# Kernel tuning notes

Measured on AMD Instinct MI355X. Metric: run time of the kernel, lower is better.

## Reference

```python
import jax, jax.numpy as jnp
import numpy as np

N_NODES = 100000


def gcn_layer(x, ei, W, b):
    # PyG GCNConv with add_self_loops=True, edge_weight=None (all ones)
    N = x.shape[0]
    loops = jnp.arange(N, dtype=ei.dtype)
    src = jnp.concatenate([ei[0], loops])
    dst = jnp.concatenate([ei[1], loops])
    h = x @ W  # [N, out_dim]
    ones = jnp.ones(src.shape[0], dtype=x.dtype)
    deg = jax.ops.segment_sum(ones, dst, num_segments=N)
    dinv = jnp.where(deg > 0, jax.lax.rsqrt(deg), 0.0)
    norm = dinv[src] * dinv[dst]  # [E+N]
    msgs = norm[:, None] * h[src]
    out = jax.ops.segment_sum(msgs, dst, num_segments=N)
    return out + b


def forward_once(x, ei, W1, b1, W2, b2):
    h = jax.nn.relu(gcn_layer(x, ei, W1, b1))
    # Dropout(0.25) is identity in eval mode
    z = gcn_layer(h, ei, W2, b2)
    return z  # [N, embed_dim]


def setup_inputs() -> dict:
    key = jax.random.key(0)
    k = jax.random.split(key, 6)
    feat_dim, hidden_dim, embed_dim = 128, 32, 16
    R, E = 4, 1600000
    x = jax.random.normal(k[0], (N_NODES, feat_dim), dtype=jnp.float32)
    eis = jax.random.randint(k[1], (R, 2, E), 0, N_NODES, dtype=jnp.int32)
    s1 = 1.0 / np.sqrt(feat_dim)
    s2 = 1.0 / np.sqrt(hidden_dim)
    W1 = jax.random.uniform(k[2], (feat_dim, hidden_dim), jnp.float32, -s1, s1)
    b1 = jax.random.uniform(k[3], (hidden_dim,), jnp.float32, -s1, s1)
    W2 = jax.random.uniform(k[4], (hidden_dim, embed_dim), jnp.float32, -s2, s2)
    b2 = jax.random.uniform(k[5], (embed_dim,), jnp.float32, -s2, s2)
    return {"x": x, "eis": eis, "W1": W1, "b1": b1, "W2": W2, "b2": b2}


def reference(x, eis, W1, b1, W2, b2):
    # vectorize the per-relation loop over the leading R axis of eis
    embeds = jax.vmap(lambda ei: forward_once(x, ei, W1, b1, W2, b2))(eis)
    # default reduce: embeds.sum(dim=2) on [R, N, embed_dim] -> [R, N]
    return embeds.sum(axis=2)
```

## Files before the change

### kernel.cpp

```cpp
#include <hip/hip_runtime.h>


constexpr int N    = 100000;
constexpr int E    = 1600000;
constexpr int R    = 4;
constexpr int FEAT = 128;
constexpr int HID  = 32;
constexpr int EMB  = 16;
constexpr int M    = R * N;
constexpr int BS   = 256;
constexpr int SH    = 9;
constexpr int BSPAN = 1 << SH;
constexpr int NBUCK = (N + BSPAN - 1) / BSPAN;
constexpr int CH    = 4096;
constexpr int EPT   = CH / BS;
constexpr int NBKr  = (E + CH - 1) / CH;
constexpr int RB    = R * NBUCK;
constexpr int CAP   = 8960;
constexpr int SPT   = (CAP + BSPAN - 1) / BSPAN;
constexpr int FIX   = 16;
constexpr int GNB   = 64;
constexpr int XPITCH = 132;

typedef _Float16 half8 __attribute__((ext_vector_type(8)));
typedef _Float16 half2v __attribute__((ext_vector_type(2)));

__global__ __launch_bounds__(BS)
void k_gemm_h0(const float* __restrict__ x, const float* __restrict__ W1,
               _Float16* __restrict__ H0h) {
    __shared__ float xs[GNB * XPITCH];
    int base = blockIdx.x * GNB;
    int tid  = threadIdx.x;
#pragma unroll
    for (int u = 0; u < 8; ++u) {
        int f = tid + u * BS;
        int n = f >> 5;
        int c = f & 31;
        if (base + n < N) {
            float4 v = ((const float4*)(x + (size_t)(base + n) * FEAT))[c];
            int p = c ^ ((n & 7) << 2);
            *(float4*)&xs[n * XPITCH + p * 4] = v;
        }
    }
    __syncthreads();
    int oct = __builtin_amdgcn_readfirstlane(tid >> 6);
    int l   = tid & 63;
    int i   = base + l;
    const float* wp = W1 + oct * 8;
    float acc[8];
#pragma unroll
    for (int kk = 0; kk < 8; ++kk) acc[kk] = 0.f;
#pragma unroll 4
    for (int c = 0; c < 32; ++c) {
        int p = c ^ ((l & 7) << 2);
        float4 xv = *(const float4*)&xs[l * XPITCH + p * 4];
        float xk[4] = {xv.x, xv.y, xv.z, xv.w};
#pragma unroll
        for (int dk = 0; dk < 4; ++dk) {
            const float* wr = wp + (c * 4 + dk) * HID;
#pragma unroll
            for (int j = 0; j < 8; ++j)
                acc[j] = fmaf(xk[dk], wr[j], acc[j]);
        }
    }
    half8 hv;
#pragma unroll
    for (int kk = 0; kk < 8; ++kk) hv[kk] = (_Float16)acc[kk];
    if (i < N) ((half8*)H0h)[i * 4 + oct] = hv;
}

__global__ void k_wrow(const float* __restrict__ W2, const float* __restrict__ b2,
                       float* __restrict__ wrowbuf, _Float16* __restrict__ Hsc) {
    int j = threadIdx.x;
    if (j < HID) {
        float s = 0.f;
#pragma unroll
        for (int k = 0; k < EMB; ++k) s += W2[j * EMB + k];
        wrowbuf[j] = s;
    } else if (j == HID) {
        float s = 0.f;
#pragma unroll
        for (int k = 0; k < EMB; ++k) s += b2[k];
        wrowbuf[HID] = s;
    } else if (j >= 34 && j < 50) {
        ((unsigned*)(Hsc + (size_t)M * HID))[j - 34] = 0u;
    }
}

__global__ void k_scat2(const int* __restrict__ eis, int* __restrict__ gcur,
                        int* __restrict__ binned) {
    __shared__ int hist[NBUCK], lstart[NBUCK], cursor[NBUCK], gbase[NBUCK];
    __shared__ int wpart[BS / 64];
    __shared__ int shuf[CH];
    __shared__ unsigned char bkt[CH];
    int r = blockIdx.x / NBKr, k = blockIdx.x - r * NBKr;
    const int* srcp = eis + (size_t)r * 2 * E;
    const int* dstp = srcp + E;
    int e0 = k * CH, n = min(CH, E - e0);
    int tid = threadIdx.x;

    int dreg[EPT], sreg[EPT];
    if (n == CH) {
#pragma unroll
        for (int u = 0; u < EPT; ++u) {
            dreg[u] = dstp[e0 + tid + u * BS];
            sreg[u] = srcp[e0 + tid + u * BS];
        }
    } else {
#pragma unroll
        for (int u = 0; u < EPT; ++u) {
            int i = tid + u * BS;
            dreg[u] = (i < n) ? dstp[e0 + i] : -1;
            sreg[u] = (i < n) ? srcp[e0 + i] : 0;
        }
    }
    for (int b = tid; b < NBUCK; b += BS) hist[b] = 0;
    __syncthreads();
#pragma unroll
    for (int u = 0; u < EPT; ++u)
        if (dreg[u] >= 0) atomicAdd(&hist[dreg[u] >> SH], 1);
    __syncthreads();
    int v = (tid < NBUCK) ? hist[tid] : 0;
    int lanei = tid & 63;
    int s = v;
#pragma unroll
    for (int d = 1; d < 64; d <<= 1) {
        int xup = __shfl_up(s, d, 64);
        s += (lanei >= d) ? xup : 0;
    }
    if (lanei == 63) wpart[tid >> 6] = s;
    __syncthreads();
    int offw = 0;
#pragma unroll
    for (int ww = 0; ww < BS / 64; ++ww)
        offw += (ww < (tid >> 6)) ? wpart[ww] : 0;
    int ex = offw + s - v;
    if (tid < NBUCK) {
        lstart[tid] = ex;
        cursor[tid] = ex;
        gbase[tid] = atomicAdd(&gcur[r * NBUCK + tid], v);
    }
    __syncthreads();
#pragma unroll
    for (int u = 0; u < EPT; ++u) {
        int d = dreg[u];
        if (d >= 0) {
            int b = d >> SH;
            int pos = atomicAdd(&cursor[b], 1);
            shuf[pos] = ((d & (BSPAN - 1)) << 17) | sreg[u];
            bkt[pos]  = (unsigned char)b;
        }
    }
    __syncthreads();
    for (int i = tid; i < n; i += BS) {
        int b = bkt[i];
        int pos = gbase[b] + (i - lstart[b]);
        if (pos < CAP)
            binned[(size_t)(r * NBUCK + b) * CAP + pos] = shuf[i];
    }
}

__global__ __launch_bounds__(BSPAN)
void k_sort3(const int* __restrict__ gcur, int* __restrict__ binned,
             int* __restrict__ off, int* __restrict__ cnt,
             float* __restrict__ dinv, const half8* __restrict__ H0h,
             half8* __restrict__ Hsc, int* __restrict__ fixedsrc) {
    __shared__ int fix_lds[FIX * BSPAN];
    __shared__ int hist[BSPAN], cur[BSPAN], exs[BSPAN];
    __shared__ int wpart[BSPAN / 64];
    int gb = blockIdx.x;
    int r = gb / NBUCK, b = gb - r * NBUCK;
    int n = min(gcur[gb], CAP);
    int base = gb * CAP;
    int tid = threadIdx.x;
    int rg[SPT];
#pragma unroll
    for (int u = 0; u < SPT; ++u) {
        int i = tid + u * BSPAN;
        rg[u] = (i < n) ? binned[base + i] : -1;
    }
    hist[tid] = 0;
    __syncthreads();
#pragma unroll
    for (int u = 0; u < SPT; ++u)
        if (rg[u] >= 0) atomicAdd(&hist[((unsigned)rg[u]) >> 17], 1);
    __syncthreads();
    int v = hist[tid];
    int lanei = tid & 63;
    int s = v;
#pragma unroll
    for (int d = 1; d < 64; d <<= 1) {
        int xup = __shfl_up(s, d, 64);
        s += (lanei >= d) ? xup : 0;
    }
    if (lanei == 63) wpart[tid >> 6] = s;
    __syncthreads();
    int offw = 0;
#pragma unroll
    for (int ww = 0; ww < BSPAN / 64; ++ww)
        offw += (ww < (tid >> 6)) ? wpart[ww] : 0;
    int ex = offw + s - v;
    cur[tid] = ex;
    exs[tid] = ex;
    int node = (b << SH) + tid;
    int ri = r * N + node;
    if (node < N) {
        off[ri] = base + ex;
        cnt[ri] = v;
        dinv[ri] = rsqrtf((float)v + 1.0f);
    }
    __syncthreads();
#pragma unroll
    for (int u = 0; u < SPT; ++u) {
        int rc = rg[u];
        if (rc >= 0) {
            int nd = ((unsigned)rc) >> 17;
            int pos = atomicAdd(&cur[nd], 1);
            int val = rc & 0x1FFFF;
            binned[base + pos] = val;
            int k = pos - exs[nd];
            if (k < FIX) fix_lds[k * BSPAN + nd] = val;
        }
    }
    __syncthreads();
    if (node < N) {
        int nn = min(v, FIX);
#pragma unroll
        for (int cc = 0; cc < 4; ++cc) {
            int4 w;
            w.x = (cc * 4 + 0 < nn) ? fix_lds[(cc * 4 + 0) * BSPAN + tid] : 0;
            w.y = (cc * 4 + 1 < nn) ? fix_lds[(cc * 4 + 1) * BSPAN + tid] : 0;
            w.z = (cc * 4 + 2 < nn) ? fix_lds[(cc * 4 + 2) * BSPAN + tid] : 0;
            w.w = (cc * 4 + 3 < nn) ? fix_lds[(cc * 4 + 3) * BSPAN + tid] : 0;
            ((int4*)(fixedsrc + (size_t)ri * FIX))[cc] = w;
        }
        float di = rsqrtf((float)v + 1.0f);
#pragma unroll
        for (int cc = 0; cc < 4; ++cc) {
            half8 h = H0h[(size_t)node * 4 + cc];
            half8 o;
#pragma unroll
            for (int kk = 0; kk < 8; ++kk) o[kk] = (_Float16)(di * (float)h[kk]);
            Hsc[(size_t)ri * 4 + cc] = o;
        }
    }
}

__global__ void k_l1(const int* __restrict__ off, const int* __restrict__ cnt,
                     const int* __restrict__ ssrc, const int* __restrict__ fixedsrc,
                     const float* __restrict__ dinv, const half8* __restrict__ Hsc,
                     const float* __restrict__ b1, const float* __restrict__ wrowbuf,
                     float* __restrict__ q) {
    int t = blockIdx.x * blockDim.x + threadIdx.x;
    int ri = t >> 4;
    if (ri >= M) return;
    int lane = t & 15;
    int c   = lane & 3;
    int sub = lane >> 2;
    int i = ri % N;
    int rbase = ri - i;
    float di = dinv[ri];
    int n = cnt[ri];
    int fs = fixedsrc[(size_t)ri * FIX + lane];
    int base = off[ri];
    half2v acc[4];
    half2v zz = {(_Float16)0.f, (_Float16)0.f};
#pragma unroll
    for (int kk = 0; kk < 4; ++kk) acc[kk] = zz;

    auto procwin = [&](int sbv, int m) {
        for (int bq = 0; bq < 4 && bq * 4 < m; ++bq) {
            int slot = bq * 4 + sub;
            int sj = __shfl(sbv, slot, 16);
            int idx = (slot < m) ? (rbase + sj) : M;
            half8 h = Hsc[(size_t)idx * 4 + c];
#pragma unroll
            for (int kk = 0; kk < 4; ++kk) {
                half2v hp = {h[2 * kk], h[2 * kk + 1]};
                acc[kk] = acc[kk] + hp;
            }
        }
    };

    int sb = (16 + lane < n) ? ssrc[base + 16 + lane] : 0;
    procwin(fs, n);
    for (int k0 = 16; k0 < n; k0 += 16) {
        int sbn = (k0 + 16 + lane < n) ? ssrc[base + k0 + 16 + lane] : 0;
        procwin(sb, n - k0);
        sb = sbn;
    }
#pragma unroll
    for (int o = 4; o <= 8; o <<= 1) {
#pragma unroll
        for (int kk = 0; kk < 4; ++kk) {
            int av = __builtin_bit_cast(int, acc[kk]);
            av = __shfl_xor(av, o, 16);
            acc[kk] = acc[kk] + __builtin_bit_cast(half2v, av);
        }
    }
    half8 hs = Hsc[(size_t)ri * 4 + c];
#pragma unroll
    for (int kk = 0; kk < 4; ++kk) {
        half2v hp = {hs[2 * kk], hs[2 * kk + 1]};
        acc[kk] = acc[kk] + hp;
    }
    float p = 0.f;
#pragma unroll
    for (int kk = 0; kk < 8; ++kk) {
        float av = (float)acc[kk >> 1][kk & 1];
        int j = c * 8 + kk;
        float h1 = fmaf(di, av, b1[j]);
        h1 = fmaxf(h1, 0.f);
        p = fmaf(h1, wrowbuf[j], p);
    }
    p += __shfl_xor(p, 1, 16);
    p += __shfl_xor(p, 2, 16);
    if (lane == 0) q[ri] = di * p;
}

__global__ void k_l2(const int* __restrict__ off, const int* __restrict__ cnt,
                     const int* __restrict__ ssrc, const int* __restrict__ fixedsrc,
                     const float* __restrict__ dinv, const float* __restrict__ q,
                     const float* __restrict__ wrowbuf, float* __restrict__ out) {
    int t = blockIdx.x * blockDim.x + threadIdx.x;
    int ri = t >> 3;
    if (ri >= M) return;
    int lane = t & 7;
    int i = ri % N;
    int rbase = ri - i;
    int n = cnt[ri];
    int f0 = fixedsrc[(size_t)ri * FIX + lane];
    int f1 = fixedsrc[(size_t)ri * FIX + 8 + lane];
    int base = off[ri];
    float val = 0.f;
    if (lane < n)     val += q[rbase + f0];
    if (8 + lane < n) val += q[rbase + f1];
    for (int idx = 16 + lane; idx < n; idx += 8) {
        int s = ssrc[base + idx];
        val += q[rbase + s];
    }
#pragma unroll
    for (int o = 4; o > 0; o >>= 1) val += __shfl_xor(val, o, 8);
    if (lane == 0)
        out[ri] = dinv[ri] * (val + q[ri]) + wrowbuf[HID];
}

extern "C" void kernel_launch(void* const* d_in, const int* in_sizes, int n_in,
                              void* d_out, int out_size, void* d_ws, size_t ws_size,
                              hipStream_t stream) {
    const float* x  = (const float*)d_in[0];
    const int*  eis = (const int*)d_in[1];
    const float* W1 = (const float*)d_in[2];
    const float* b1 = (const float*)d_in[3];
    const float* W2 = (const float*)d_in[4];
    const float* b2 = (const float*)d_in[5];
    float* out = (float*)d_out;

    _Float16* H0h = (_Float16*)d_ws;
    float* dinv   = (float*)d_ws + (size_t)N * HID / 2;
    float* q      = dinv + M;
    int*   off    = (int*)(q + M);
    int*   cnt    = off + M;
    float* wrowbuf = (float*)(cnt + M);
    int*   gcur   = (int*)(wrowbuf + 64);
    int*   binned = gcur + RB;
    _Float16* Hsc = (_Float16*)(binned + (size_t)RB * CAP);
    int* fixedsrc = (int*)(Hsc + (size_t)(M + 1) * HID);

    k_gemm_h0<<<(N + GNB - 1) / GNB, BS, 0, stream>>>(x, W1, H0h);
    k_wrow  <<<1, 64, 0, stream>>>(W2, b2, wrowbuf, Hsc);
    hipMemsetAsync(gcur, 0, (size_t)RB * sizeof(int), stream);
    k_scat2 <<<R * NBKr, BS, 0, stream>>>(eis, gcur, binned);
    k_sort3 <<<RB, BSPAN, 0, stream>>>(gcur, binned, off, cnt, dinv,
                                       (const half8*)H0h, (half8*)Hsc, fixedsrc);
    k_l1    <<<(M * 16 + BS - 1) / BS, BS, 0, stream>>>(off, cnt, binned, fixedsrc,
                                                        dinv, (const half8*)Hsc, b1,
                                                        wrowbuf, q);
    k_l2    <<<(M * 8 + BS - 1) / BS, BS, 0, stream>>>(off, cnt, binned, fixedsrc,
                                                       dinv, q, wrowbuf, out);
}
```

Baseline: 335.1 us.

## Replace two-pass bucket sort with global-atomic histogram, scan, and direct scatter

Builds the per-destination adjacency with a global atomic histogram over destinations, a per-bucket scan that records overflow offsets beyond a fixed 16-slot inline list, and a second pass that places each source with a global atomic cursor. The first FIX sources go straight into fixedsrc and only the overflow goes into a much smaller binned array. This drops the LDS-heavy shuffle and the in-bucket sort kernel and shrinks workspace traffic. In exchange it adds two M-sized memsets, issues many scattered global atomics, and makes neighbor order nondeterministic; overflow is capped per bucket.

```diff
diff --git a/kernel.cpp b/kernel.cpp
--- a/kernel.cpp
+++ b/kernel.cpp
@@ -16,8 +16,7 @@
 constexpr int EPT   = CH / BS;
 constexpr int NBKr  = (E + CH - 1) / CH;
 constexpr int RB    = R * NBUCK;
-constexpr int CAP   = 8960;
-constexpr int SPT   = (CAP + BSPAN - 1) / BSPAN;
+constexpr int OCAP  = 1536;
 constexpr int FIX   = 16;
 constexpr int GNB   = 64;
 constexpr int XPITCH = 132;
@@ -87,18 +86,78 @@
     }
 }
 
-__global__ void k_scat2(const int* __restrict__ eis, int* __restrict__ gcur,
-                        int* __restrict__ binned) {
-    __shared__ int hist[NBUCK], lstart[NBUCK], cursor[NBUCK], gbase[NBUCK];
-    __shared__ int wpart[BS / 64];
-    __shared__ int shuf[CH];
-    __shared__ unsigned char bkt[CH];
+__global__ void k_hist(const int* __restrict__ eis, int* __restrict__ cnt) {
+    int r = blockIdx.x / NBKr, k = blockIdx.x - r * NBKr;
+    const int* dstp = eis + (size_t)r * 2 * E + E;
+    int e0 = k * CH, n = min(CH, E - e0);
+    int tid = threadIdx.x;
+    int dreg[EPT];
+    if (n == CH) {
+#pragma unroll
+        for (int u = 0; u < EPT; ++u) dreg[u] = dstp[e0 + tid + u * BS];
+    } else {
+#pragma unroll
+        for (int u = 0; u < EPT; ++u) {
+            int i = tid + u * BS;
+            dreg[u] = (i < n) ? dstp[e0 + i] : -1;
+        }
+    }
+    int* c = cnt + (size_t)r * N;
+#pragma unroll
+    for (int u = 0; u < EPT; ++u)
+        if (dreg[u] >= 0) atomicAdd(&c[dreg[u]], 1);
+}
+
+__global__ __launch_bounds__(BSPAN)
+void k_scan(int* __restrict__ cnt, int* __restrict__ ovoff,
+            float* __restrict__ dinv, const half8* __restrict__ H0h,
+            half8* __restrict__ Hsc) {
+    __shared__ int wpart[BSPAN / 64];
+    int gb = blockIdx.x;
+    int r = gb / NBUCK, b = gb - r * NBUCK;
+    int tid = threadIdx.x;
+    int node = (b << SH) + tid;
+    int ri = r * N + node;
+    int d = 0, v = 0;
+    if (node < N) { d = cnt[ri]; v = max(d - FIX, 0); }
+    int lanei = tid & 63;
+    int s = v;
+#pragma unroll
+    for (int dd = 1; dd < 64; dd <<= 1) {
+        int xup = __shfl_up(s, dd, 64);
+        s += (lanei >= dd) ? xup : 0;
+    }
+    if (lanei == 63) wpart[tid >> 6] = s;
+    __syncthreads();
+    int offw = 0;
+#pragma unroll
+    for (int ww = 0; ww < BSPAN / 64; ++ww)
+        offw += (ww < (tid >> 6)) ? wpart[ww] : 0;
+    int ex = offw + s - v;
+    if (node < N) {
+        ovoff[ri] = gb * OCAP + ex;
+        cnt[ri] = min(d, FIX + max(OCAP - ex, 0));
+        float di = rsqrtf((float)d + 1.0f);
+        dinv[ri] = di;
+#pragma unroll
+        for (int cc = 0; cc < 4; ++cc) {
+            half8 h = H0h[(size_t)node * 4 + cc];
+            half8 o;
+#pragma unroll
+            for (int kk = 0; kk < 8; ++kk) o[kk] = (_Float16)(di * (float)h[kk]);
+            Hsc[(size_t)ri * 4 + cc] = o;
+        }
+    }
+}
+
+__global__ void k_scat(const int* __restrict__ eis, int* __restrict__ cur,
+                       const int* __restrict__ ovoff, int* __restrict__ fixedsrc,
+                       int* __restrict__ binned) {
     int r = blockIdx.x / NBKr, k = blockIdx.x - r * NBKr;
     const int* srcp = eis + (size_t)r * 2 * E;
     const int* dstp = srcp + E;
     int e0 = k * CH, n = min(CH, E - e0);
     int tid = threadIdx.x;
-
     int dreg[EPT], sreg[EPT];
     if (n == CH) {
 #pragma unroll
@@ -114,140 +173,26 @@
             sreg[u] = (i < n) ? srcp[e0 + i] : 0;
         }
     }
-    for (int b = tid; b < NBUCK; b += BS) hist[b] = 0;
-    __syncthreads();
-#pragma unroll
-    for (int u = 0; u < EPT; ++u)
-        if (dreg[u] >= 0) atomicAdd(&hist[dreg[u] >> SH], 1);
-    __syncthreads();
-    int v = (tid < NBUCK) ? hist[tid] : 0;
-    int lanei = tid & 63;
-    int s = v;
-#pragma unroll
-    for (int d = 1; d < 64; d <<= 1) {
-        int xup = __shfl_up(s, d, 64);
-        s += (lanei >= d) ? xup : 0;
-    }
-    if (lanei == 63) wpart[tid >> 6] = s;
-    __syncthreads();
-    int offw = 0;
-#pragma unroll
-    for (int ww = 0; ww < BS / 64; ++ww)
-        offw += (ww < (tid >> 6)) ? wpart[ww] : 0;
-    int ex = offw + s - v;
-    if (tid < NBUCK) {
-        lstart[tid] = ex;
-        cursor[tid] = ex;
-        gbase[tid] = atomicAdd(&gcur[r * NBUCK + tid], v);
-    }
-    __syncthreads();
+    int* cu = cur + (size_t)r * N;
 #pragma unroll
     for (int u = 0; u < EPT; ++u) {
         int d = dreg[u];
         if (d >= 0) {
-            int b = d >> SH;
-            int pos = atomicAdd(&cursor[b], 1);
-            shuf[pos] = ((d & (BSPAN - 1)) << 17) | sreg[u];
-            bkt[pos]  = (unsigned char)b;
-        }
-    }
-    __syncthreads();
-    for (int i = tid; i < n; i += BS) {
-        int b = bkt[i];
-        int pos = gbase[b] + (i - lstart[b]);
-        if (pos < CAP)
-            binned[(size_t)(r * NBUCK + b) * CAP + pos] = shuf[i];
-    }
-}
-
-__global__ __launch_bounds__(BSPAN)
-void k_sort3(const int* __restrict__ gcur, int* __restrict__ binned,
-             int* __restrict__ off, int* __restrict__ cnt,
-             float* __restrict__ dinv, const half8* __restrict__ H0h,
-             half8* __restrict__ Hsc, int* __restrict__ fixedsrc) {
-    __shared__ int fix_lds[FIX * BSPAN];
-    __shared__ int hist[BSPAN], cur[BSPAN], exs[BSPAN];
-    __shared__ int wpart[BSPAN / 64];
-    int gb = blockIdx.x;
-    int r = gb / NBUCK, b = gb - r * NBUCK;
-    int n = min(gcur[gb], CAP);
-    int base = gb * CAP;
-    int tid = threadIdx.x;
-    int rg[SPT];
-#pragma unroll
-    for (int u = 0; u < SPT; ++u) {
-        int i = tid + u * BSPAN;
-        rg[u] = (i < n) ? binned[base + i] : -1;
-    }
-    hist[tid] = 0;
-    __syncthreads();
-#pragma unroll
-    for (int u = 0; u < SPT; ++u)
-        if (rg[u] >= 0) atomicAdd(&hist[((unsigned)rg[u]) >> 17], 1);
-    __syncthreads();
-    int v = hist[tid];
-    int lanei = tid & 63;
-    int s = v;
-#pragma unroll
-    for (int d = 1; d < 64; d <<= 1) {
-        int xup = __shfl_up(s, d, 64);
-        s += (lanei >= d) ? xup : 0;
-    }
-    if (lanei == 63) wpart[tid >> 6] = s;
-    __syncthreads();
-    int offw = 0;
-#pragma unroll
-    for (int ww = 0; ww < BSPAN / 64; ++ww)
-        offw += (ww < (tid >> 6)) ? wpart[ww] : 0;
-    int ex = offw + s - v;
-    cur[tid] = ex;
-    exs[tid] = ex;
-    int node = (b << SH) + tid;
-    int ri = r * N + node;
-    if (node < N) {
-        off[ri] = base + ex;
-        cnt[ri] = v;
-        dinv[ri] = rsqrtf((float)v + 1.0f);
-    }
-    __syncthreads();
-#pragma unroll
-    for (int u = 0; u < SPT; ++u) {
-        int rc = rg[u];
-        if (rc >= 0) {
-            int nd = ((unsigned)rc) >> 17;
-            int pos = atomicAdd(&cur[nd], 1);
-            int val = rc & 0x1FFFF;
-            binned[base + pos] = val;
-            int k = pos - exs[nd];
-            if (k < FIX) fix_lds[k * BSPAN + nd] = val;
-        }
-    }
-    __syncthreads();
-    if (node < N) {
-        int nn = min(v, FIX);
-#pragma unroll
-        for (int cc = 0; cc < 4; ++cc) {
-            int4 w;
-            w.x = (cc * 4 + 0 < nn) ? fix_lds[(cc * 4 + 0) * BSPAN + tid] : 0;
-            w.y = (cc * 4 + 1 < nn) ? fix_lds[(cc * 4 + 1) * BSPAN + tid] : 0;
-            w.z = (cc * 4 + 2 < nn) ? fix_lds[(cc * 4 + 2) * BSPAN + tid] : 0;
-            w.w = (cc * 4 + 3 < nn) ? fix_lds[(cc * 4 + 3) * BSPAN + tid] : 0;
-            ((int4*)(fixedsrc + (size_t)ri * FIX))[cc] = w;
-        }
-        float di = rsqrtf((float)v + 1.0f);
-#pragma unroll
-        for (int cc = 0; cc < 4; ++cc) {
-            half8 h = H0h[(size_t)node * 4 + cc];
-            half8 o;
-#pragma unroll
-            for (int kk = 0; kk < 8; ++kk) o[kk] = (_Float16)(di * (float)h[kk]);
-            Hsc[(size_t)ri * 4 + cc] = o;
-        }
-    }
-}
-
-__global__ void k_l1(const int* __restrict__ off, const int* __restrict__ cnt,
-                     const int* __restrict__ ssrc, const int* __restrict__ fixedsrc,
+            int ri = r * N + d;
+            int kk = atomicAdd(&cu[d], 1);
+            if (kk < FIX) {
+                fixedsrc[(size_t)ri * FIX + kk] = sreg[u];
+            } else {
+                int pos = ovoff[ri] + kk - FIX;
+                int gb = r * NBUCK + (d >> SH);
+                if (pos < (gb + 1) * OCAP) binned[pos] = sreg[u];
+            }
+        }
+    }
+}
+
+__global__ void k_l1(const int* __restrict__ cnt, const int* __restrict__ ssrc,
+                     const int* __restrict__ fixedsrc, const int* __restrict__ ovoff,
                      const float* __restrict__ dinv, const half8* __restrict__ Hsc,
                      const float* __restrict__ b1, const float* __restrict__ wrowbuf,
                      float* __restrict__ q) {
@@ -262,7 +207,7 @@
     float di = dinv[ri];
     int n = cnt[ri];
     int fs = fixedsrc[(size_t)ri * FIX + lane];
-    int base = off[ri];
+    int base = ovoff[ri] - FIX;
     half2v acc[4];
     half2v zz = {(_Float16)0.f, (_Float16)0.f};
 #pragma unroll
@@ -318,8 +263,8 @@
     if (lane == 0) q[ri] = di * p;
 }
 
-__global__ void k_l2(const int* __restrict__ off, const int* __restrict__ cnt,
-                     const int* __restrict__ ssrc, const int* __restrict__ fixedsrc,
+__global__ void k_l2(const int* __restrict__ cnt, const int* __restrict__ ssrc,
+                     const int* __restrict__ fixedsrc, const int* __restrict__ ovoff,
                      const float* __restrict__ dinv, const float* __restrict__ q,
                      const float* __restrict__ wrowbuf, float* __restrict__ out) {
     int t = blockIdx.x * blockDim.x + threadIdx.x;
@@ -331,7 +276,7 @@
     int n = cnt[ri];
     int f0 = fixedsrc[(size_t)ri * FIX + lane];
     int f1 = fixedsrc[(size_t)ri * FIX + 8 + lane];
-    int base = off[ri];
+    int base = ovoff[ri] - FIX;
     float val = 0.f;
     if (lane < n)     val += q[rbase + f0];
     if (8 + lane < n) val += q[rbase + f1];
@@ -359,23 +304,26 @@
     _Float16* H0h = (_Float16*)d_ws;
     float* dinv   = (float*)d_ws + (size_t)N * HID / 2;
     float* q      = dinv + M;
-    int*   off    = (int*)(q + M);
-    int*   cnt    = off + M;
-    float* wrowbuf = (float*)(cnt + M);
-    int*   gcur   = (int*)(wrowbuf + 64);
-    int*   binned = gcur + RB;
-    _Float16* Hsc = (_Float16*)(binned + (size_t)RB * CAP);
+    int*   cnt    = (int*)(q + M);
+    int*   cur    = cnt + M;
+    int*   ovoff  = cur + M;
+    float* wrowbuf = (float*)(ovoff + M);
+    int*   binned = (int*)(wrowbuf + 64);
+    _Float16* Hsc = (_Float16*)(binned + (size_t)RB * OCAP);
     int* fixedsrc = (int*)(Hsc + (size_t)(M + 1) * HID);
 
+    hipMemsetAsync(cnt, 0, (size_t)M * sizeof(int), stream);
+    hipMemsetAsync(cur, 0, (size_t)M * sizeof(int), stream);
     k_gemm_h0<<<(N + GNB - 1) / GNB, BS, 0, stream>>>(x, W1, H0h);
     k_wrow  <<<1, 64, 0, stream>>>(W2, b2, wrowbuf, Hsc);
-    hipMemsetAsync(gcur, 0, (size_t)RB * sizeof(int), stream);
-    k_scat2 <<<R * NBKr, BS, 0, stream>>>(eis, gcur, binned);
-    k_sort3 <<<RB, BSPAN, 0, stream>>>(gcur, binned, off, cnt, dinv,
-                                       (const half8*)H0h, (half8*)Hsc, fixedsrc);
-    k_l1    <<<(M * 16 + BS - 1) / BS, BS, 0, stream>>>(off, cnt, binned, fixedsrc,
-                                                        dinv, (const half8*)Hsc, b1,
+    k_hist  <<<R * NBKr, BS, 0, stream>>>(eis, cnt);
+    k_scan  <<<RB, BSPAN, 0, stream>>>(cnt, ovoff, dinv, (const half8*)H0h,
+                                       (half8*)Hsc);
+    k_scat  <<<R * NBKr, BS, 0, stream>>>(eis, cur, ovoff, fixedsrc, binned);
+    k_l1    <<<(M * 16 + BS - 1) / BS, BS, 0, stream>>>(cnt, binned, fixedsrc,
+                                                        ovoff, dinv,
+                                                        (const half8*)Hsc, b1,
                                                         wrowbuf, q);
-    k_l2    <<<(M * 8 + BS - 1) / BS, BS, 0, stream>>>(off, cnt, binned, fixedsrc,
-                                                       dinv, q, wrowbuf, out);
-}
+    k_l2    <<<(M * 8 + BS - 1) / BS, BS, 0, stream>>>(cnt, binned, fixedsrc,
+                                                       ovoff, dinv, q, wrowbuf, out);
+}
```

New measurement: 1.013 ms. +202.3%, slower.
